# Kernel tuning notes

Measured on AMD Instinct MI355X. Metric: run time of the kernel, lower is better.

Reference implementation:

```python
import jax, jax.numpy as jnp
import numpy as np

N_NODES = 65536
N_EDGES = 1048576
IN_F = 128
HID_F = 128
OUT_F = 128


def setup_inputs() -> dict:
    key = jax.random.key(0)
    ks = jax.random.split(key, 8)
    feat = jax.random.normal(ks[0], (N_NODES, IN_F), dtype=jnp.float32)
    eweight = jax.random.uniform(ks[1], (N_EDGES, 1), dtype=jnp.float32)
    W1 = jax.random.normal(ks[2], (IN_F, HID_F), dtype=jnp.float32) * (1.0 / np.sqrt(IN_F))
    b1 = jnp.zeros((HID_F,), dtype=jnp.float32)
    W2 = jax.random.normal(ks[3], (HID_F, OUT_F), dtype=jnp.float32) * (1.0 / np.sqrt(HID_F))
    b2 = jnp.zeros((OUT_F,), dtype=jnp.float32)
    src = jax.random.randint(ks[4], (N_EDGES,), 0, N_NODES, dtype=jnp.int32)
    dst = jax.random.randint(ks[5], (N_EDGES,), 0, N_NODES, dtype=jnp.int32)
    return {"feat": feat, "eweight": eweight, "W1": W1, "b1": b1,
            "W2": W2, "b2": b2, "src": src, "dst": dst}


def _degrees(src, dst, n_nodes):
    ones = jnp.ones(src.shape[0], dtype=jnp.float32)
    deg_out = jax.ops.segment_sum(ones, src, num_segments=n_nodes)
    deg_in = jax.ops.segment_sum(ones, dst, num_segments=n_nodes)
    # DGL GraphConv clamps degree to min 1 before norm='both'
    return jnp.clip(deg_out, 1.0, None), jnp.clip(deg_in, 1.0, None)


def _graph_conv(feat, W, b, src, dst, out_norm, in_norm, n_nodes):
    # DGL GraphConv, norm='both': D_out^{-1/2} x -> x W -> spmm sum -> D_in^{-1/2} -> + b
    h = feat * out_norm[:, None]
    h = h @ W
    agg = jax.ops.segment_sum(h[src], dst, num_segments=n_nodes)
    return agg * in_norm[:, None] + b


def reference(feat, eweight, W1, b1, W2, b2, src, dst):
    n = feat.shape[0]
    deg_out, deg_in = _degrees(src, dst, n)
    out_norm = jax.lax.rsqrt(deg_out)
    in_norm = jax.lax.rsqrt(deg_in)
    h = _graph_conv(feat, W1, b1, src, dst, out_norm, in_norm, n)
    h = jax.nn.relu(h)
    h = _graph_conv(h, W2, b2, src, dst, out_norm, in_norm, n)
    # final update_all: u_mul_e + sum (eweight given)
    msg = h[src] * eweight  # [E, OUT_F]
    return jax.ops.segment_sum(msg, dst, num_segments=n)
```

## Files before the change

kernel.cpp:

```cpp
#include <hip/hip_runtime.h>

#define F 128
#define NN 65536
#define NBA 512
#define NBS 128
#define COARSE 256
#define CAP_BIN 4864
#define CAP_CSR 5632

typedef unsigned int uint;
typedef unsigned short ushort;
typedef unsigned char uchar;
typedef __attribute__((ext_vector_type(8))) short short8;
typedef __attribute__((ext_vector_type(8))) unsigned short ushort8;
typedef __attribute__((ext_vector_type(4))) float floatx4;

__device__ __forceinline__ ushort f2bf(float f) {
  uint u = __float_as_uint(f);
  u += 0x7fffu + ((u >> 16) & 1u);
  return (ushort)(u >> 16);
}


__global__ __launch_bounds__(256) void w_prep(const float* __restrict__ W1,
                                              const float* __restrict__ W2,
                                              ushort* __restrict__ W1t,
                                              ushort* __restrict__ W2t,
                                              int* __restrict__ cursorD,
                                              int* __restrict__ cursorS) {
  int b = blockIdx.x;
  if (b == 0) cursorD[threadIdx.x] = 0;
  if (b == 1) cursorS[threadIdx.x] = 0;
  const float* W = (b < 64) ? W1 : W2;
  ushort* Wt = (b < 64) ? W1t : W2t;
  int idx = (b & 63) * 256 + threadIdx.x;
  int k = idx >> 7, n = idx & 127;
  Wt[n * F + k] = f2bf(W[idx]);
}

__global__ __launch_bounds__(256) void bin_edges(
    const int* __restrict__ src, const int* __restrict__ dst,
    const float* __restrict__ ew, int E,
    int* __restrict__ cursorD, int* __restrict__ cursorS,
    uint2* __restrict__ slotD, uchar* __restrict__ srcF) {
  __shared__ int cnt[4][COARSE];
  __shared__ int base[COARSE];
  bool isD = blockIdx.x < NBA;
  int blk = isD ? blockIdx.x : blockIdx.x - NBA;
  int nblk = isD ? NBA : NBS;
  const int* key = isD ? dst : src;
  int* cursor = isD ? cursorD : cursorS;
  int wave = threadIdx.x >> 6;
  for (int i = threadIdx.x; i < 4 * COARSE; i += 256) ((int*)cnt)[i] = 0;
  __syncthreads();
  int chunk = (E + nblk - 1) / nblk;
  int s0 = blk * chunk, s1 = min(E, s0 + chunk);
  for (int i = s0 + threadIdx.x; i < s1; i += 256)
    atomicAdd(&cnt[wave][key[i] >> 8], 1);
  __syncthreads();
  if (threadIdx.x < COARSE) {
    int b = threadIdx.x;
    int tot = cnt[0][b] + cnt[1][b] + cnt[2][b] + cnt[3][b];
    base[b] = tot ? atomicAdd(&cursor[b], tot) : 0;
    cnt[0][b] = 0;
  }
  __syncthreads();
  if (isD) {
    for (int i = s0 + threadIdx.x; i < s1; i += 256) {
      int d = dst[i];
      int bin = d >> 8;
      int p = base[bin] + atomicAdd(&cnt[0][bin], 1);
      if (p < CAP_BIN) {
        uint2 v;
        v.x = (uint)(src[i] & 0xffff) | ((uint)f2bf(ew[i]) << 16);
        v.y = (uint)(d & 255);
        slotD[(size_t)bin * CAP_BIN + p] = v;
      }
    }
  } else {
    for (int i = s0 + threadIdx.x; i < s1; i += 256) {
      int s = src[i];
      int bin = s >> 8;
      int p = base[bin] + atomicAdd(&cnt[0][bin], 1);
      if (p < CAP_BIN) srcF[(size_t)bin * CAP_BIN + p] = (uchar)(s & 255);
    }
  }
}

__global__ __launch_bounds__(1024) void bucket_csr(
    const uint2* __restrict__ slotD, const int* __restrict__ cursorD,
    int2* __restrict__ rowRange, float* __restrict__ inNorm, uint* __restrict__ csr,
    const uchar* __restrict__ srcF, const int* __restrict__ cursorS,
    float* __restrict__ outNorm) {
  __shared__ int hist[256], base[256], cur[256];
  int t = threadIdx.x;
  if (blockIdx.x >= COARSE) {
    int b = blockIdx.x - COARSE;
    int lo = b * CAP_BIN;
    int cntS = min(cursorS[b], CAP_BIN);
    if (t < 256) hist[t] = 0;
    __syncthreads();
    for (int i = lo + t; i < lo + cntS; i += 1024)
      atomicAdd(&hist[srcF[i]], 1);
    __syncthreads();
    if (t < 256) outNorm[b * 256 + t] = rsqrtf((float)max(hist[t], 1));
    return;
  }
  int b = blockIdx.x;
  int lo = b * CAP_BIN;
  int cntD = min(cursorD[b], CAP_BIN);
  int hi = lo + cntD;
  if (t < 256) hist[t] = 0;
  __syncthreads();
  for (int i = lo + t; i < hi; i += 1024)
    atomicAdd(&hist[slotD[i].y], 1);
  __syncthreads();
  if (t < 256) base[t] = (hist[t] + 3) & ~3;
  __syncthreads();
  for (int off = 1; off < 256; off <<= 1) {
    int x = 0;
    if (t < 256 && t >= off) x = base[t - off];
    __syncthreads();
    if (t < 256) base[t] += x;
    __syncthreads();
  }
  if (t < 256) {
    int v = hist[t];
    int sz4 = (v + 3) & ~3;
    int st = b * CAP_CSR + base[t] - sz4;
    base[t] = st;
    cur[t] = 0;
    int node = b * 256 + t;
    rowRange[node] = make_int2(st, v);
    inNorm[node] = rsqrtf((float)max(v, 1));
    for (int p = st + v; p < st + sz4; ++p) csr[p] = 0x80000000u;
  }
  __syncthreads();
  for (int i = lo + t; i < hi; i += 1024) {
    uint2 v = slotD[i];
    int fine = v.y;
    int p = base[fine] + atomicAdd(&cur[fine], 1);
    csr[p] = v.x;
  }
}

template <bool BF16IN>
__global__ __launch_bounds__(256) void gemm_mfma(
    const void* __restrict__ Xv, const float* __restrict__ scale,
    const ushort* __restrict__ Wt, ushort* __restrict__ Y) {
  __shared__ ushort sA[128 * 136];
  __shared__ ushort sB[128 * 136];
  int t = threadIdx.x;
  int row0 = blockIdx.x * 128;

  {
    int r = t >> 1, hf = t & 1;
    ushort* ap = sA + r * 136 + hf * 64;
    if (BF16IN) {
      const ushort* xp = (const ushort*)Xv;
#pragma unroll
      for (int j = 0; j < 8; ++j) {
        int q = 2 * hf + (j >> 2);
        *(ushort8*)(ap + j * 8) =
            *(const ushort8*)(xp + ((size_t)q * NN + row0 + r) * 32 + (j & 3) * 8);
      }
    } else {
      const float* xp = (const float*)Xv + (size_t)(row0 + r) * F + hf * 64;
      float s = scale[row0 + r];
#pragma unroll
      for (int j = 0; j < 8; ++j) {
        float4 v0 = *(const float4*)(xp + j * 8);
        float4 v1 = *(const float4*)(xp + j * 8 + 4);
        ushort8 o;
        o[0] = f2bf(v0.x * s); o[1] = f2bf(v0.y * s); o[2] = f2bf(v0.z * s); o[3] = f2bf(v0.w * s);
        o[4] = f2bf(v1.x * s); o[5] = f2bf(v1.y * s); o[6] = f2bf(v1.z * s); o[7] = f2bf(v1.w * s);
        *(ushort8*)(ap + j * 8) = o;
      }
    }
  }
  {
    int n = t >> 1, hf = t & 1;
    const ushort* wp = Wt + n * F + hf * 64;
    ushort* bp = sB + n * 136 + hf * 64;
#pragma unroll
    for (int j = 0; j < 8; ++j)
      *(ushort8*)(bp + j * 8) = *(const ushort8*)(wp + j * 8);
  }
  __syncthreads();

  int lane = t & 63, wave = t >> 6;
  int quad = lane >> 4, l16 = lane & 15;
  int mrow0 = wave * 32;

  floatx4 acc[2][8];
#pragma unroll
  for (int a = 0; a < 2; ++a)
#pragma unroll
    for (int c = 0; c < 8; ++c) acc[a][c] = (floatx4){0.f, 0.f, 0.f, 0.f};

#pragma unroll
  for (int kc = 0; kc < 128; kc += 32) {
    short8 afrag[2], bfrag[8];
#pragma unroll
    for (int a = 0; a < 2; ++a)
      afrag[a] = *(const short8*)(sA + (mrow0 + a * 16 + l16) * 136 + kc + quad * 8);
#pragma unroll
    for (int c = 0; c < 8; ++c)
      bfrag[c] = *(const short8*)(sB + (c * 16 + l16) * 136 + kc + quad * 8);
#pragma unroll
    for (int a = 0; a < 2; ++a)
#pragma unroll
      for (int c = 0; c < 8; ++c)
        acc[a][c] = __builtin_amdgcn_mfma_f32_16x16x32_bf16(afrag[a], bfrag[c], acc[a][c], 0, 0, 0);
  }

#pragma unroll
  for (int a = 0; a < 2; ++a)
#pragma unroll
    for (int c = 0; c < 8; ++c)
#pragma unroll
      for (int r = 0; r < 4; ++r) {
        int row = row0 + mrow0 + a * 16 + quad * 4 + r;
        int col = c * 16 + l16;
        Y[((size_t)(col >> 5) * NN + row) * 32 + (col & 31)] = f2bf(acc[a][c][r]);
      }
}


template <bool EW, bool NB, bool RELU, bool PS, bool OUT_BF16>
__global__ __launch_bounds__(256) void spmm(
    const ushort* __restrict__ hb, const int2* __restrict__ rowRange,
    const uint* __restrict__ csr, const float* __restrict__ inNorm,
    const float* __restrict__ bias, const float* __restrict__ postScale,
    void* __restrict__ outv) {
  int bid = blockIdx.x;
  int plane = (bid & 7) >> 1;
  int chunk = ((bid >> 3) << 1) | (bid & 1);
  int lane = threadIdx.x & 63;
  int g = lane >> 2;
  int j = lane & 3;
  int n = chunk * 64 + (threadIdx.x >> 6) * 16 + g;
  int2 r = rowRange[n];
  int len4 = (r.y + 3) & ~3;
  const char* pb = (const char*)hb + (size_t)plane * ((size_t)NN * 64);
  uint joff = (uint)j << 4;
  float acc[8] = {0.f, 0.f, 0.f, 0.f, 0.f, 0.f, 0.f, 0.f};

#define GQ(e, c, q)                                                      \
  {                                                                      \
    uint ei = (e);                                                       \
    c = *(const uint4*)(pb + (((ei & 0xffffu) << 6) | joff));            \
    q = EW ? __uint_as_float(ei & 0xffff0000u)                           \
           : ((int)ei >= 0 ? 1.0f : 0.0f);                               \
  }
#define ACC8(c, q)                                                      \
  {                                                                     \
    acc[0] = fmaf(__uint_as_float(c.x << 16), q, acc[0]);               \
    acc[1] = fmaf(__uint_as_float(c.x & 0xffff0000u), q, acc[1]);       \
    acc[2] = fmaf(__uint_as_float(c.y << 16), q, acc[2]);               \
    acc[3] = fmaf(__uint_as_float(c.y & 0xffff0000u), q, acc[3]);       \
    acc[4] = fmaf(__uint_as_float(c.z << 16), q, acc[4]);               \
    acc[5] = fmaf(__uint_as_float(c.z & 0xffff0000u), q, acc[5]);       \
    acc[6] = fmaf(__uint_as_float(c.w << 16), q, acc[6]);               \
    acc[7] = fmaf(__uint_as_float(c.w & 0xffff0000u), q, acc[7]);       \
  }

  int i = 0;
  while (i + 8 <= len4) {
    uint4 e0 = *(const uint4*)(csr + r.x + i);
    uint4 e1 = *(const uint4*)(csr + r.x + i + 4);
    uint4 c0, c1, c2, c3, c4, c5, c6, c7;
    float q0, q1, q2, q3, q4, q5, q6, q7;
    GQ(e0.x, c0, q0) GQ(e0.y, c1, q1) GQ(e0.z, c2, q2) GQ(e0.w, c3, q3)
    GQ(e1.x, c4, q4) GQ(e1.y, c5, q5) GQ(e1.z, c6, q6) GQ(e1.w, c7, q7)
    ACC8(c0, q0) ACC8(c1, q1) ACC8(c2, q2) ACC8(c3, q3)
    ACC8(c4, q4) ACC8(c5, q5) ACC8(c6, q6) ACC8(c7, q7)
    i += 8;
  }
  if (i < len4) {
    uint4 e0 = *(const uint4*)(csr + r.x + i);
    uint4 c0, c1, c2, c3;
    float q0, q1, q2, q3;
    GQ(e0.x, c0, q0) GQ(e0.y, c1, q1) GQ(e0.z, c2, q2) GQ(e0.w, c3, q3)
    ACC8(c0, q0) ACC8(c1, q1) ACC8(c2, q2) ACC8(c3, q3)
  }
#undef GQ
#undef ACC8

  if (NB) {
    float sc = inNorm[n];
    float4 b0 = ((const float4*)bias)[plane * 8 + j * 2];
    float4 b1 = ((const float4*)bias)[plane * 8 + j * 2 + 1];
    float bb[8] = {b0.x, b0.y, b0.z, b0.w, b1.x, b1.y, b1.z, b1.w};
#pragma unroll
    for (int k = 0; k < 8; ++k) {
      acc[k] = fmaf(acc[k], sc, bb[k]);
      if (RELU) acc[k] = fmaxf(acc[k], 0.f);
    }
    if (PS) {
      float o = postScale[n];
#pragma unroll
      for (int k = 0; k < 8; ++k) acc[k] *= o;
    }
  }
  if (OUT_BF16) {
    uint4 o;
    o.x = ((uint)f2bf(acc[1]) << 16) | (uint)f2bf(acc[0]);
    o.y = ((uint)f2bf(acc[3]) << 16) | (uint)f2bf(acc[2]);
    o.z = ((uint)f2bf(acc[5]) << 16) | (uint)f2bf(acc[4]);
    o.w = ((uint)f2bf(acc[7]) << 16) | (uint)f2bf(acc[6]);
    ((uint4*)outv)[((size_t)plane * NN + n) * 4 + j] = o;
  } else {
    float4 lo = {acc[0], acc[1], acc[2], acc[3]};
    float4 hi = {acc[4], acc[5], acc[6], acc[7]};
    ((float4*)outv)[(size_t)n * 32 + plane * 8 + j * 2] = lo;
    ((float4*)outv)[(size_t)n * 32 + plane * 8 + j * 2 + 1] = hi;
  }
}


extern "C" void kernel_launch(void* const* d_in, const int* in_sizes, int n_in,
                              void* d_out, int out_size, void* d_ws, size_t ws_size,
                              hipStream_t stream) {
  const float* feat = (const float*)d_in[0];
  const float* ew   = (const float*)d_in[1];
  const float* W1   = (const float*)d_in[2];
  const float* b1   = (const float*)d_in[3];
  const float* W2   = (const float*)d_in[4];
  const float* b2   = (const float*)d_in[5];
  const int*   src  = (const int*)d_in[6];
  const int*   dst  = (const int*)d_in[7];
  const int N = in_sizes[0] / F;
  const int E = in_sizes[6];
  float* out = (float*)d_out;

  char* ws = (char*)d_ws;
  size_t off = 0;
  auto alloc = [&](size_t bytes) {
    void* p = ws + off;
    off += (bytes + 255) & ~(size_t)255;
    return p;
  };
  int2*   rowRange = (int2*)alloc((size_t)N * 8);
  float*  inNorm   = (float*)alloc((size_t)N * 4);
  float*  outNorm  = (float*)alloc((size_t)N * 4);
  ushort* W1t      = (ushort*)alloc((size_t)F * F * 2);
  ushort* W2t      = (ushort*)alloc((size_t)F * F * 2);
  int*    cursorD  = (int*)alloc(COARSE * 4);
  int*    cursorS  = (int*)alloc(COARSE * 4);
  uint*   csr      = (uint*)alloc((size_t)COARSE * CAP_CSR * 4);
  ushort* bufAb    = (ushort*)alloc((size_t)N * F * 2);
  ushort* bufBb    = (ushort*)alloc((size_t)N * F * 2);
  ushort* bufCb    = (ushort*)alloc((size_t)N * F * 2);
  if (off > ws_size) return;

  uint2* slotD;
  uchar* srcF;
  {
    char* tp = (char*)bufBb;
    size_t toff = 0;
    auto talloc = [&](size_t bytes) {
      void* p = tp + toff;
      toff += (bytes + 255) & ~(size_t)255;
      return p;
    };
    slotD = (uint2*)talloc((size_t)COARSE * CAP_BIN * 8);
    srcF  = (uchar*)talloc((size_t)COARSE * CAP_BIN);
  }

  w_prep<<<128, 256, 0, stream>>>(W1, W2, W1t, W2t, cursorD, cursorS);
  bin_edges<<<NBA + NBS, 256, 0, stream>>>(src, dst, ew, E, cursorD, cursorS, slotD, srcF);
  bucket_csr<<<2 * COARSE, 1024, 0, stream>>>(slotD, cursorD, rowRange, inNorm, csr,
                                              srcF, cursorS, outNorm);

  gemm_mfma<false><<<N / 128, 256, 0, stream>>>(feat, outNorm, W1t, bufAb);
  spmm<false, true, true, true, true><<<N / 16, 256, 0, stream>>>(
      bufAb, rowRange, csr, inNorm, b1, outNorm, bufBb);
  gemm_mfma<true><<<N / 128, 256, 0, stream>>>(bufBb, nullptr, W2t, bufAb);
  spmm<false, true, false, false, true><<<N / 16, 256, 0, stream>>>(
      bufAb, rowRange, csr, inNorm, b2, nullptr, bufCb);
  spmm<true, false, false, false, false><<<N / 16, 256, 0, stream>>>(
      bufCb, rowRange, csr, nullptr, nullptr, nullptr, out);
}
```

Baseline: 264.8 us.

## Use XCC-aware persistent SpMM with atomic per-plane work queues and nontemporal access

The SpMM kernels become persistent. Each workgroup reads its XCC ID from a hardware register to choose a feature plane, so each plane's gathered rows stay in one XCD's L2. Each wavefront then pulls 16-row chunks from an atomic per-plane counter, which balances load across rows of different length. CSR loads and output stores use nontemporal hints so streaming data does not evict gathered features from cache. The risks are that correctness depends on the hardware dispatching workgroups to all 8 XCCs (otherwise a plane's queue is never drained), and that atomics add contention.

```diff
diff --git a/kernel.cpp b/kernel.cpp
--- a/kernel.cpp
+++ b/kernel.cpp
@@ -2,6 +2,7 @@
 
 #define F 128
 #define NN 65536
+#define NCHUNK (NN / 16)
 #define NBA 512
 #define NBS 128
 #define COARSE 256
@@ -14,6 +15,7 @@
 typedef __attribute__((ext_vector_type(8))) short short8;
 typedef __attribute__((ext_vector_type(8))) unsigned short ushort8;
 typedef __attribute__((ext_vector_type(4))) float floatx4;
+typedef __attribute__((ext_vector_type(4))) uint uintx4;
 
 __device__ __forceinline__ ushort f2bf(float f) {
   uint u = __float_as_uint(f);
@@ -27,10 +29,12 @@
                                               ushort* __restrict__ W1t,
                                               ushort* __restrict__ W2t,
                                               int* __restrict__ cursorD,
-                                              int* __restrict__ cursorS) {
+                                              int* __restrict__ cursorS,
+                                              int* __restrict__ planeQ) {
   int b = blockIdx.x;
   if (b == 0) cursorD[threadIdx.x] = 0;
   if (b == 1) cursorS[threadIdx.x] = 0;
+  if (b == 2 && threadIdx.x < 16) planeQ[threadIdx.x] = 0;
   const float* W = (b < 64) ? W1 : W2;
   ushort* Wt = (b < 64) ? W1t : W2t;
   int idx = (b & 63) * 256 + threadIdx.x;
@@ -232,90 +236,103 @@
     const ushort* __restrict__ hb, const int2* __restrict__ rowRange,
     const uint* __restrict__ csr, const float* __restrict__ inNorm,
     const float* __restrict__ bias, const float* __restrict__ postScale,
-    void* __restrict__ outv) {
-  int bid = blockIdx.x;
-  int plane = (bid & 7) >> 1;
-  int chunk = ((bid >> 3) << 1) | (bid & 1);
+    void* __restrict__ outv, int* __restrict__ q) {
+  uint xcc;
+  asm volatile("s_getreg_b32 %0, hwreg(HW_REG_XCC_ID)" : "=s"(xcc));
+  int plane = (int)((xcc & 7u) >> 1);
   int lane = threadIdx.x & 63;
   int g = lane >> 2;
   int j = lane & 3;
-  int n = chunk * 64 + (threadIdx.x >> 6) * 16 + g;
-  int2 r = rowRange[n];
-  int len4 = (r.y + 3) & ~3;
   const char* pb = (const char*)hb + (size_t)plane * ((size_t)NN * 64);
   uint joff = (uint)j << 4;
-  float acc[8] = {0.f, 0.f, 0.f, 0.f, 0.f, 0.f, 0.f, 0.f};
-
-#define GQ(e, c, q)                                                      \
+  int* qp = q + plane;
+
+  float bb[8];
+  if (NB) {
+    float4 b0 = ((const float4*)bias)[plane * 8 + j * 2];
+    float4 b1 = ((const float4*)bias)[plane * 8 + j * 2 + 1];
+    bb[0] = b0.x; bb[1] = b0.y; bb[2] = b0.z; bb[3] = b0.w;
+    bb[4] = b1.x; bb[5] = b1.y; bb[6] = b1.z; bb[7] = b1.w;
+  }
+
+#define GQ(e, c, q_)                                                     \
   {                                                                      \
     uint ei = (e);                                                       \
     c = *(const uint4*)(pb + (((ei & 0xffffu) << 6) | joff));            \
-    q = EW ? __uint_as_float(ei & 0xffff0000u)                           \
-           : ((int)ei >= 0 ? 1.0f : 0.0f);                               \
-  }
-#define ACC8(c, q)                                                      \
+    q_ = EW ? __uint_as_float(ei & 0xffff0000u)                          \
+            : ((int)ei >= 0 ? 1.0f : 0.0f);                              \
+  }
+#define ACC8(c, q_)                                                     \
   {                                                                     \
-    acc[0] = fmaf(__uint_as_float(c.x << 16), q, acc[0]);               \
-    acc[1] = fmaf(__uint_as_float(c.x & 0xffff0000u), q, acc[1]);       \
-    acc[2] = fmaf(__uint_as_float(c.y << 16), q, acc[2]);               \
-    acc[3] = fmaf(__uint_as_float(c.y & 0xffff0000u), q, acc[3]);       \
-    acc[4] = fmaf(__uint_as_float(c.z << 16), q, acc[4]);               \
-    acc[5] = fmaf(__uint_as_float(c.z & 0xffff0000u), q, acc[5]);       \
-    acc[6] = fmaf(__uint_as_float(c.w << 16), q, acc[6]);               \
-    acc[7] = fmaf(__uint_as_float(c.w & 0xffff0000u), q, acc[7]);       \
-  }
-
-  int i = 0;
-  while (i + 8 <= len4) {
-    uint4 e0 = *(const uint4*)(csr + r.x + i);
-    uint4 e1 = *(const uint4*)(csr + r.x + i + 4);
-    uint4 c0, c1, c2, c3, c4, c5, c6, c7;
-    float q0, q1, q2, q3, q4, q5, q6, q7;
-    GQ(e0.x, c0, q0) GQ(e0.y, c1, q1) GQ(e0.z, c2, q2) GQ(e0.w, c3, q3)
-    GQ(e1.x, c4, q4) GQ(e1.y, c5, q5) GQ(e1.z, c6, q6) GQ(e1.w, c7, q7)
-    ACC8(c0, q0) ACC8(c1, q1) ACC8(c2, q2) ACC8(c3, q3)
-    ACC8(c4, q4) ACC8(c5, q5) ACC8(c6, q6) ACC8(c7, q7)
-    i += 8;
-  }
-  if (i < len4) {
-    uint4 e0 = *(const uint4*)(csr + r.x + i);
-    uint4 c0, c1, c2, c3;
-    float q0, q1, q2, q3;
-    GQ(e0.x, c0, q0) GQ(e0.y, c1, q1) GQ(e0.z, c2, q2) GQ(e0.w, c3, q3)
-    ACC8(c0, q0) ACC8(c1, q1) ACC8(c2, q2) ACC8(c3, q3)
+    acc[0] = fmaf(__uint_as_float(c.x << 16), q_, acc[0]);              \
+    acc[1] = fmaf(__uint_as_float(c.x & 0xffff0000u), q_, acc[1]);      \
+    acc[2] = fmaf(__uint_as_float(c.y << 16), q_, acc[2]);              \
+    acc[3] = fmaf(__uint_as_float(c.y & 0xffff0000u), q_, acc[3]);      \
+    acc[4] = fmaf(__uint_as_float(c.z << 16), q_, acc[4]);              \
+    acc[5] = fmaf(__uint_as_float(c.z & 0xffff0000u), q_, acc[5]);      \
+    acc[6] = fmaf(__uint_as_float(c.w << 16), q_, acc[6]);              \
+    acc[7] = fmaf(__uint_as_float(c.w & 0xffff0000u), q_, acc[7]);      \
+  }
+
+  for (;;) {
+    int chunk = 0;
+    if (lane == 0) chunk = atomicAdd(qp, 1);
+    chunk = __shfl(chunk, 0, 64);
+    if (chunk >= NCHUNK) break;
+    int n = chunk * 16 + g;
+    int2 r = rowRange[n];
+    int len4 = (r.y + 3) & ~3;
+    float acc[8] = {0.f, 0.f, 0.f, 0.f, 0.f, 0.f, 0.f, 0.f};
+
+    int i = 0;
+    while (i + 8 <= len4) {
+      uintx4 e0 = __builtin_nontemporal_load((const uintx4*)(csr + r.x + i));
+      uintx4 e1 = __builtin_nontemporal_load((const uintx4*)(csr + r.x + i + 4));
+      uint4 c0, c1, c2, c3, c4, c5, c6, c7;
+      float q0, q1, q2, q3, q4, q5, q6, q7;
+      GQ(e0.x, c0, q0) GQ(e0.y, c1, q1) GQ(e0.z, c2, q2) GQ(e0.w, c3, q3)
+      GQ(e1.x, c4, q4) GQ(e1.y, c5, q5) GQ(e1.z, c6, q6) GQ(e1.w, c7, q7)
+      ACC8(c0, q0) ACC8(c1, q1) ACC8(c2, q2) ACC8(c3, q3)
+      ACC8(c4, q4) ACC8(c5, q5) ACC8(c6, q6) ACC8(c7, q7)
+      i += 8;
+    }
+    if (i < len4) {
+      uintx4 e0 = __builtin_nontemporal_load((const uintx4*)(csr + r.x + i));
+      uint4 c0, c1, c2, c3;
+      float q0, q1, q2, q3;
+      GQ(e0.x, c0, q0) GQ(e0.y, c1, q1) GQ(e0.z, c2, q2) GQ(e0.w, c3, q3)
+      ACC8(c0, q0) ACC8(c1, q1) ACC8(c2, q2) ACC8(c3, q3)
+    }
+
+    if (NB) {
+      float sc = inNorm[n];
+#pragma unroll
+      for (int k = 0; k < 8; ++k) {
+        acc[k] = fmaf(acc[k], sc, bb[k]);
+        if (RELU) acc[k] = fmaxf(acc[k], 0.f);
+      }
+      if (PS) {
+        float o = postScale[n];
+#pragma unroll
+        for (int k = 0; k < 8; ++k) acc[k] *= o;
+      }
+    }
+    if (OUT_BF16) {
+      uintx4 o;
+      o.x = ((uint)f2bf(acc[1]) << 16) | (uint)f2bf(acc[0]);
+      o.y = ((uint)f2bf(acc[3]) << 16) | (uint)f2bf(acc[2]);
+      o.z = ((uint)f2bf(acc[5]) << 16) | (uint)f2bf(acc[4]);
+      o.w = ((uint)f2bf(acc[7]) << 16) | (uint)f2bf(acc[6]);
+      __builtin_nontemporal_store(o, (uintx4*)outv + ((size_t)plane * NN + n) * 4 + j);
+    } else {
+      floatx4 lo = {acc[0], acc[1], acc[2], acc[3]};
+      floatx4 hi = {acc[4], acc[5], acc[6], acc[7]};
+      __builtin_nontemporal_store(lo, (floatx4*)outv + (size_t)n * 32 + plane * 8 + j * 2);
+      __builtin_nontemporal_store(hi, (floatx4*)outv + (size_t)n * 32 + plane * 8 + j * 2 + 1);
+    }
   }
 #undef GQ
 #undef ACC8
-
-  if (NB) {
-    float sc = inNorm[n];
-    float4 b0 = ((const float4*)bias)[plane * 8 + j * 2];
-    float4 b1 = ((const float4*)bias)[plane * 8 + j * 2 + 1];
-    float bb[8] = {b0.x, b0.y, b0.z, b0.w, b1.x, b1.y, b1.z, b1.w};
-#pragma unroll
-    for (int k = 0; k < 8; ++k) {
-      acc[k] = fmaf(acc[k], sc, bb[k]);
-      if (RELU) acc[k] = fmaxf(acc[k], 0.f);
-    }
-    if (PS) {
-      float o = postScale[n];
-#pragma unroll
-      for (int k = 0; k < 8; ++k) acc[k] *= o;
-    }
-  }
-  if (OUT_BF16) {
-    uint4 o;
-    o.x = ((uint)f2bf(acc[1]) << 16) | (uint)f2bf(acc[0]);
-    o.y = ((uint)f2bf(acc[3]) << 16) | (uint)f2bf(acc[2]);
-    o.z = ((uint)f2bf(acc[5]) << 16) | (uint)f2bf(acc[4]);
-    o.w = ((uint)f2bf(acc[7]) << 16) | (uint)f2bf(acc[6]);
-    ((uint4*)outv)[((size_t)plane * NN + n) * 4 + j] = o;
-  } else {
-    float4 lo = {acc[0], acc[1], acc[2], acc[3]};
-    float4 hi = {acc[4], acc[5], acc[6], acc[7]};
-    ((float4*)outv)[(size_t)n * 32 + plane * 8 + j * 2] = lo;
-    ((float4*)outv)[(size_t)n * 32 + plane * 8 + j * 2 + 1] = hi;
-  }
 }
 
 
@@ -348,6 +365,7 @@
   ushort* W2t      = (ushort*)alloc((size_t)F * F * 2);
   int*    cursorD  = (int*)alloc(COARSE * 4);
   int*    cursorS  = (int*)alloc(COARSE * 4);
+  int*    planeQ   = (int*)alloc(16 * 4);
   uint*   csr      = (uint*)alloc((size_t)COARSE * CAP_CSR * 4);
   ushort* bufAb    = (ushort*)alloc((size_t)N * F * 2);
   ushort* bufBb    = (ushort*)alloc((size_t)N * F * 2);
@@ -368,17 +386,17 @@
     srcF  = (uchar*)talloc((size_t)COARSE * CAP_BIN);
   }
 
-  w_prep<<<128, 256, 0, stream>>>(W1, W2, W1t, W2t, cursorD, cursorS);
+  w_prep<<<128, 256, 0, stream>>>(W1, W2, W1t, W2t, cursorD, cursorS, planeQ);
   bin_edges<<<NBA + NBS, 256, 0, stream>>>(src, dst, ew, E, cursorD, cursorS, slotD, srcF);
   bucket_csr<<<2 * COARSE, 1024, 0, stream>>>(slotD, cursorD, rowRange, inNorm, csr,
                                               srcF, cursorS, outNorm);
 
   gemm_mfma<false><<<N / 128, 256, 0, stream>>>(feat, outNorm, W1t, bufAb);
-  spmm<false, true, true, true, true><<<N / 16, 256, 0, stream>>>(
-      bufAb, rowRange, csr, inNorm, b1, outNorm, bufBb);
+  spmm<false, true, true, true, true><<<2048, 256, 0, stream>>>(
+      bufAb, rowRange, csr, inNorm, b1, outNorm, bufBb, planeQ);
   gemm_mfma<true><<<N / 128, 256, 0, stream>>>(bufBb, nullptr, W2t, bufAb);
-  spmm<false, true, false, false, true><<<N / 16, 256, 0, stream>>>(
-      bufAb, rowRange, csr, inNorm, b2, nullptr, bufCb);
-  spmm<true, false, false, false, false><<<N / 16, 256, 0, stream>>>(
-      bufCb, rowRange, csr, nullptr, nullptr, nullptr, out);
-}
+  spmm<false, true, false, false, true><<<2048, 256, 0, stream>>>(
+      bufAb, rowRange, csr, inNorm, b2, nullptr, bufCb, planeQ + 4);
+  spmm<true, false, false, false, false><<<2048, 256, 0, stream>>>(
+      bufCb, rowRange, csr, nullptr, nullptr, nullptr, out, planeQ + 8);
+}
```

After: 1.023 ms. 3.86x slower.
